# Kernel tuning notes

Hardware: AMD Instinct MI355X
Metric: run time of the kernel (lower is better)

The kernel has to match this reference:

```python
import jax, jax.numpy as jnp
import numpy as np

EPS_COS = 1e-16   # epsilon added to operands (as in the torch module)
EPS_NRM = 1e-8    # torch cosine_similarity clamps norms at 1e-8


def setup_inputs() -> dict:
    key = jax.random.key(0)
    k0, k1, k2, k3, k4, k5 = jax.random.split(key, 6)
    B, N, M = 64, 2048, 256
    stdev = 1.0 / np.sqrt(N + M)
    memory = jax.random.uniform(k0, (B, N, M), jnp.float32, -stdev, stdev)
    k = jax.random.normal(k1, (B, M), jnp.float32)
    g = jax.random.uniform(k2, (B, 1), jnp.float32)
    gamma = jax.random.uniform(k3, (1,), jnp.float32)
    # w_prev[:,0] = w_u_prev, w_prev[:,1] = w_r_prev (positive weightings)
    w_prev = jax.random.uniform(k4, (B, 2, N), jnp.float32)
    # w_lu_prev is a 0/1 least-recently-used mask
    w_lu_prev = jax.random.randint(k5, (B, N), 0, 2, jnp.int32)
    return {"memory": memory, "k": k, "g": g, "gamma": gamma,
            "w_prev": w_prev, "w_lu_prev": w_lu_prev, "n": 4}


def reference(memory, k, g, gamma, w_prev, w_lu_prev, n):
    # --- _similarity: softmax over cosine similarity along memory slots ---
    mem_e = memory + EPS_COS                      # [B, N, M]
    k_e = k[:, None, :] + EPS_COS                 # [B, 1, M]
    num = jnp.einsum('bnm,bom->bn', mem_e, k_e)   # [B, N]
    mem_nrm = jnp.maximum(jnp.linalg.norm(mem_e, axis=-1), EPS_NRM)
    k_nrm = jnp.maximum(jnp.linalg.norm(k_e, axis=-1), EPS_NRM)  # [B, 1]
    w_r = jax.nn.softmax(num / (mem_nrm * k_nrm), axis=-1)       # [B, N]

    # --- interpolate write weighting and usage weighting ---
    w_u_prev = w_prev[:, 0]                        # [B, N]
    w_r_prev = w_prev[:, 1]                        # [B, N]
    w_lu_prev_f = w_lu_prev.astype(memory.dtype)   # [B, N], 0/1 mask
    w_w = g * w_r_prev + (1.0 - g) * w_lu_prev_f   # [B, N]
    w_u = gamma * w_u_prev + w_r + w_w             # [B, N]

    # --- least-used mask: w_u <= n-th smallest usage (per batch) ---
    nth_smallest = jnp.sort(w_u, axis=1)[:, n - 1]           # [B]
    w_lu = (w_u <= nth_smallest[:, None]).astype(memory.dtype)  # [B, N]

    # --- zero out slots that were least-recently-used last step ---
    mem_zeroed = memory * (1.0 - w_lu_prev_f)[..., None]      # [B, N, M]

    # --- lrua_write: rank-1 outer-product write, then read with w_r ---
    mem_new = mem_zeroed + w_w[..., None] * k[:, None, :]     # [B, N, M]
    read = jnp.einsum('bn,bnm->bm', w_r, mem_new)             # [B, M]
    return read
```

## Files before the change

kernel.cpp:

```cpp
#include <hip/hip_runtime.h>
#include <math.h>

#define EPS_COS 1e-16f
#define EPS_NRM 1e-8f

constexpr int B = 64;
constexpr int N = 2048;
constexpr int M = 256;

constexpr int BLK    = 512;
constexpr int WAVES  = BLK / 64;
constexpr int CHUNK  = 256;
constexpr int ROWS   = CHUNK / WAVES;
constexpr int NCHUNK = N / CHUNK;

__global__ __launch_bounds__(BLK)
void k1_fused(const float* __restrict__ mem,
              const float* __restrict__ kk,
              const float* __restrict__ g,
              const float* __restrict__ w_prev,
              const int*   __restrict__ lu_prev,
              float* __restrict__ pread,
              float* __restrict__ pZ,
              float* __restrict__ pS1)
{
    const int b    = blockIdx.y;
    const int c    = blockIdx.x;
    const int tid  = threadIdx.x;
    const int w    = tid >> 6;
    const int lane = tid & 63;
    const int n0   = c * CHUNK;

    float4 kv = *reinterpret_cast<const float4*>(kk + (size_t)b * M + lane * 4);
    kv.x += EPS_COS; kv.y += EPS_COS; kv.z += EPS_COS; kv.w += EPS_COS;
    float ksq = kv.x*kv.x + kv.y*kv.y + kv.z*kv.z + kv.w*kv.w;
#pragma unroll
    for (int off = 32; off; off >>= 1) ksq += __shfl_xor(ksq, off);
    const float kn = fmaxf(sqrtf(ksq), EPS_NRM);

    const float gb   = g[b];
    const float* wrp = w_prev + (size_t)b * 2 * N + N;
    const int*   lup = lu_prev + (size_t)b * N;
    const float* base = mem + ((size_t)b * N + n0 + w) * M + lane * 4;

    float4 acc = make_float4(0.f, 0.f, 0.f, 0.f);
    float Zp = 0.f, s1p = 0.f;

    auto process = [&](int i, const float4& v) {
        float m0 = v.x + EPS_COS, m1 = v.y + EPS_COS;
        float m2 = v.z + EPS_COS, m3 = v.w + EPS_COS;
        float dot = m0*kv.x + m1*kv.y + m2*kv.z + m3*kv.w;
        float msq = m0*m0 + m1*m1 + m2*m2 + m3*m3;
#pragma unroll
        for (int off = 32; off; off >>= 1) {
            dot += __shfl_xor(dot, off);
            msq += __shfl_xor(msq, off);
        }
        const int n = n0 + w + WAVES * i;
        const float cosv = dot / (fmaxf(sqrtf(msq), EPS_NRM) * kn);
        const float e  = __expf(cosv);
        const float lu = (float)lup[n];
        const float ww = gb * wrp[n] + (1.f - gb) * lu;
        Zp += e;
        s1p = fmaf(e, ww, s1p);
        const float cw = e * (1.f - lu);
        acc.x = fmaf(cw, v.x, acc.x);
        acc.y = fmaf(cw, v.y, acc.y);
        acc.z = fmaf(cw, v.z, acc.z);
        acc.w = fmaf(cw, v.w, acc.w);
    };

    float4 cur = *reinterpret_cast<const float4*>(base);
#pragma unroll 4
    for (int i = 0; i < ROWS - 1; ++i) {
        float4 nxt = *reinterpret_cast<const float4*>(base + (size_t)(i + 1) * WAVES * M);
        process(i, cur);
        cur = nxt;
    }
    process(ROWS - 1, cur);

    __shared__ float sred[WAVES * M];
    __shared__ float sZ[WAVES], sS1[WAVES];
    *reinterpret_cast<float4*>(&sred[w * M + lane * 4]) = acc;
    if (lane == 0) { sZ[w] = Zp; sS1[w] = s1p; }
    __syncthreads();

    if (tid < M) {
        float r = 0.f;
#pragma unroll
        for (int q = 0; q < WAVES; ++q) r += sred[q * M + tid];
        pread[((size_t)b * NCHUNK + c) * M + tid] = r;
    }
    if (tid == 0) {
        float z = 0.f, s = 0.f;
#pragma unroll
        for (int q = 0; q < WAVES; ++q) { z += sZ[q]; s += sS1[q]; }
        pZ[b * NCHUNK + c]  = z;
        pS1[b * NCHUNK + c] = s;
    }
}

__global__ __launch_bounds__(M)
void k2_final(const float* __restrict__ pread,
              const float* __restrict__ pZ,
              const float* __restrict__ pS1,
              const float* __restrict__ kk,
              float* __restrict__ out)
{
    const int b = blockIdx.x;
    const int t = threadIdx.x;

    __shared__ float sZ, sS1;
    if (t < 64) {
        float z = (t < NCHUNK) ? pZ[b * NCHUNK + t]  : 0.f;
        float s = (t < NCHUNK) ? pS1[b * NCHUNK + t] : 0.f;
#pragma unroll
        for (int off = 32; off; off >>= 1) {
            z += __shfl_xor(z, off);
            s += __shfl_xor(s, off);
        }
        if (t == 0) { sZ = z; sS1 = s; }
    }
    __syncthreads();

    const float invZ = 1.f / sZ;
    const float* pr = pread + (size_t)b * NCHUNK * M + t;
    float sum = 0.f;
#pragma unroll
    for (int c2 = 0; c2 < NCHUNK; ++c2) sum += pr[(size_t)c2 * M];

    out[(size_t)b * M + t] = (sum + sS1 * kk[(size_t)b * M + t]) * invZ;
}

extern "C" void kernel_launch(void* const* d_in, const int* in_sizes, int n_in,
                              void* d_out, int out_size, void* d_ws, size_t ws_size,
                              hipStream_t stream) {
    const float* mem     = (const float*)d_in[0];
    const float* kk      = (const float*)d_in[1];
    const float* g       = (const float*)d_in[2];
    const float* w_prev  = (const float*)d_in[4];
    const int*   lu_prev = (const int*)  d_in[5];
    float* out = (float*)d_out;

    float* pread = (float*)d_ws;
    float* pZ    = pread + (size_t)B * NCHUNK * M;
    float* pS1   = pZ + (size_t)B * NCHUNK;

    dim3 g1(NCHUNK, B);
    k1_fused<<<g1, BLK, 0, stream>>>(mem, kk, g, w_prev, lu_prev, pread, pZ, pS1);
    k2_final<<<B, M, 0, stream>>>(pread, pZ, pS1, kk, out);
}
```

Baseline: 29.70 us.

## Process two rows per wave with half-wave splits and deeper prefetch

Each wave now splits into two 32-lane halves that each handle a full 256-float row with two float4 loads. This cuts the butterfly shuffle reduction from six steps to five per row and processes two rows per iteration. The block shrinks to 256 threads with 128-row chunks, which doubles the grid and partial outputs, and the software prefetch goes two pairs deep. The cost is more registers, an extra cross-half reduction at the end, and more partials for the final kernel to sum.

After: 29.42 us. About the same (-0.9%).

```diff
diff --git a/kernel.cpp b/kernel.cpp
--- a/kernel.cpp
+++ b/kernel.cpp
@@ -8,10 +8,11 @@
 constexpr int N = 2048;
 constexpr int M = 256;
 
-constexpr int BLK    = 512;
+constexpr int BLK    = 256;
 constexpr int WAVES  = BLK / 64;
-constexpr int CHUNK  = 256;
-constexpr int ROWS   = CHUNK / WAVES;
+constexpr int CHUNK  = 128;
+constexpr int RPW    = CHUNK / WAVES;
+constexpr int PAIRS  = RPW / 2;
 constexpr int NCHUNK = N / CHUNK;
 
 __global__ __launch_bounds__(BLK)
@@ -29,34 +30,45 @@
     const int tid  = threadIdx.x;
     const int w    = tid >> 6;
     const int lane = tid & 63;
-    const int n0   = c * CHUNK;
+    const int half = lane >> 5;
+    const int sub  = lane & 31;
 
-    float4 kv = *reinterpret_cast<const float4*>(kk + (size_t)b * M + lane * 4);
-    kv.x += EPS_COS; kv.y += EPS_COS; kv.z += EPS_COS; kv.w += EPS_COS;
-    float ksq = kv.x*kv.x + kv.y*kv.y + kv.z*kv.z + kv.w*kv.w;
+    float4 ka = *reinterpret_cast<const float4*>(kk + (size_t)b * M + sub * 4);
+    float4 kb = *reinterpret_cast<const float4*>(kk + (size_t)b * M + 128 + sub * 4);
+    ka.x += EPS_COS; ka.y += EPS_COS; ka.z += EPS_COS; ka.w += EPS_COS;
+    kb.x += EPS_COS; kb.y += EPS_COS; kb.z += EPS_COS; kb.w += EPS_COS;
+    float ksq = ka.x*ka.x + ka.y*ka.y + ka.z*ka.z + ka.w*ka.w
+              + kb.x*kb.x + kb.y*kb.y + kb.z*kb.z + kb.w*kb.w;
 #pragma unroll
-    for (int off = 32; off; off >>= 1) ksq += __shfl_xor(ksq, off);
+    for (int off = 16; off; off >>= 1) ksq += __shfl_xor(ksq, off);
     const float kn = fmaxf(sqrtf(ksq), EPS_NRM);
 
     const float gb   = g[b];
     const float* wrp = w_prev + (size_t)b * 2 * N + N;
     const int*   lup = lu_prev + (size_t)b * N;
-    const float* base = mem + ((size_t)b * N + n0 + w) * M + lane * 4;
 
-    float4 acc = make_float4(0.f, 0.f, 0.f, 0.f);
+    const int rowbase = c * CHUNK + w * RPW;
+    const float* p = mem + ((size_t)b * N + rowbase + half) * M + sub * 4;
+
+    float4 accA = make_float4(0.f, 0.f, 0.f, 0.f);
+    float4 accB = make_float4(0.f, 0.f, 0.f, 0.f);
     float Zp = 0.f, s1p = 0.f;
 
-    auto process = [&](int i, const float4& v) {
-        float m0 = v.x + EPS_COS, m1 = v.y + EPS_COS;
-        float m2 = v.z + EPS_COS, m3 = v.w + EPS_COS;
-        float dot = m0*kv.x + m1*kv.y + m2*kv.z + m3*kv.w;
-        float msq = m0*m0 + m1*m1 + m2*m2 + m3*m3;
+    auto process = [&](int i, const float4& va, const float4& vb) {
+        float a0 = va.x + EPS_COS, a1 = va.y + EPS_COS;
+        float a2 = va.z + EPS_COS, a3 = va.w + EPS_COS;
+        float b0 = vb.x + EPS_COS, b1 = vb.y + EPS_COS;
+        float b2 = vb.z + EPS_COS, b3 = vb.w + EPS_COS;
+        float dot = a0*ka.x + a1*ka.y + a2*ka.z + a3*ka.w
+                  + b0*kb.x + b1*kb.y + b2*kb.z + b3*kb.w;
+        float msq = a0*a0 + a1*a1 + a2*a2 + a3*a3
+                  + b0*b0 + b1*b1 + b2*b2 + b3*b3;
 #pragma unroll
-        for (int off = 32; off; off >>= 1) {
+        for (int off = 16; off; off >>= 1) {
             dot += __shfl_xor(dot, off);
             msq += __shfl_xor(msq, off);
         }
-        const int n = n0 + w + WAVES * i;
+        const int n = rowbase + 2 * i + half;
         const float cosv = dot / (fmaxf(sqrtf(msq), EPS_NRM) * kn);
         const float e  = __expf(cosv);
         const float lu = (float)lup[n];
@@ -64,24 +76,44 @@
         Zp += e;
         s1p = fmaf(e, ww, s1p);
         const float cw = e * (1.f - lu);
-        acc.x = fmaf(cw, v.x, acc.x);
-        acc.y = fmaf(cw, v.y, acc.y);
-        acc.z = fmaf(cw, v.z, acc.z);
-        acc.w = fmaf(cw, v.w, acc.w);
+        accA.x = fmaf(cw, va.x, accA.x);
+        accA.y = fmaf(cw, va.y, accA.y);
+        accA.z = fmaf(cw, va.z, accA.z);
+        accA.w = fmaf(cw, va.w, accA.w);
+        accB.x = fmaf(cw, vb.x, accB.x);
+        accB.y = fmaf(cw, vb.y, accB.y);
+        accB.z = fmaf(cw, vb.z, accB.z);
+        accB.w = fmaf(cw, vb.w, accB.w);
     };
 
-    float4 cur = *reinterpret_cast<const float4*>(base);
-#pragma unroll 4
-    for (int i = 0; i < ROWS - 1; ++i) {
-        float4 nxt = *reinterpret_cast<const float4*>(base + (size_t)(i + 1) * WAVES * M);
-        process(i, cur);
-        cur = nxt;
+    float4 va0 = *reinterpret_cast<const float4*>(p);
+    float4 vb0 = *reinterpret_cast<const float4*>(p + 128);
+    float4 va1 = *reinterpret_cast<const float4*>(p + 2 * M);
+    float4 vb1 = *reinterpret_cast<const float4*>(p + 2 * M + 128);
+#pragma unroll 2
+    for (int i = 0; i < PAIRS - 2; ++i) {
+        float4 va2 = *reinterpret_cast<const float4*>(p + (size_t)(i + 2) * 2 * M);
+        float4 vb2 = *reinterpret_cast<const float4*>(p + (size_t)(i + 2) * 2 * M + 128);
+        process(i, va0, vb0);
+        va0 = va1; vb0 = vb1;
+        va1 = va2; vb1 = vb2;
     }
-    process(ROWS - 1, cur);
+    process(PAIRS - 2, va0, vb0);
+    process(PAIRS - 1, va1, vb1);
+
+    accA.x += __shfl_xor(accA.x, 32); accA.y += __shfl_xor(accA.y, 32);
+    accA.z += __shfl_xor(accA.z, 32); accA.w += __shfl_xor(accA.w, 32);
+    accB.x += __shfl_xor(accB.x, 32); accB.y += __shfl_xor(accB.y, 32);
+    accB.z += __shfl_xor(accB.z, 32); accB.w += __shfl_xor(accB.w, 32);
+    Zp  += __shfl_xor(Zp, 32);
+    s1p += __shfl_xor(s1p, 32);
 
     __shared__ float sred[WAVES * M];
     __shared__ float sZ[WAVES], sS1[WAVES];
-    *reinterpret_cast<float4*>(&sred[w * M + lane * 4]) = acc;
+    if (half == 0) {
+        *reinterpret_cast<float4*>(&sred[w * M + sub * 4])       = accA;
+        *reinterpret_cast<float4*>(&sred[w * M + 128 + sub * 4]) = accB;
+    }
     if (lane == 0) { sZ[w] = Zp; sS1[w] = s1p; }
     __syncthreads();
 
```

## Shrink chunks to 64 rows, give each wave contiguous rows with deeper prefetch

Applied to the files above, without the earlier changes.

The first kernel now uses 256-thread blocks over 64-row chunks, so the grid grows from 512 to 2048 blocks. Each wave walks 16 contiguous rows instead of interleaved rows, with a 4-deep register prefetch pipeline. The final kernel has every thread read all 32 partial Z/S1 values directly instead of doing a shared-memory reduction and a barrier. This aims to improve occupancy and memory-level parallelism on the bandwidth-bound pass, at the cost of 4x more partial sums to write and reduce.

New measurement: 34.16 us. +15.0%, slower.

```diff
diff --git a/kernel.cpp b/kernel.cpp
--- a/kernel.cpp
+++ b/kernel.cpp
@@ -8,10 +8,10 @@
 constexpr int N = 2048;
 constexpr int M = 256;
 
-constexpr int BLK    = 512;
+constexpr int BLK    = 256;
 constexpr int WAVES  = BLK / 64;
-constexpr int CHUNK  = 256;
-constexpr int ROWS   = CHUNK / WAVES;
+constexpr int CHUNK  = 64;
+constexpr int RPW    = CHUNK / WAVES;
 constexpr int NCHUNK = N / CHUNK;
 
 __global__ __launch_bounds__(BLK)
@@ -29,7 +29,6 @@
     const int tid  = threadIdx.x;
     const int w    = tid >> 6;
     const int lane = tid & 63;
-    const int n0   = c * CHUNK;
 
     float4 kv = *reinterpret_cast<const float4*>(kk + (size_t)b * M + lane * 4);
     kv.x += EPS_COS; kv.y += EPS_COS; kv.z += EPS_COS; kv.w += EPS_COS;
@@ -41,7 +40,9 @@
     const float gb   = g[b];
     const float* wrp = w_prev + (size_t)b * 2 * N + N;
     const int*   lup = lu_prev + (size_t)b * N;
-    const float* base = mem + ((size_t)b * N + n0 + w) * M + lane * 4;
+
+    const int rowbase = c * CHUNK + w * RPW;
+    const float* p = mem + ((size_t)b * N + rowbase) * M + lane * 4;
 
     float4 acc = make_float4(0.f, 0.f, 0.f, 0.f);
     float Zp = 0.f, s1p = 0.f;
@@ -56,7 +57,7 @@
             dot += __shfl_xor(dot, off);
             msq += __shfl_xor(msq, off);
         }
-        const int n = n0 + w + WAVES * i;
+        const int n = rowbase + i;
         const float cosv = dot / (fmaxf(sqrtf(msq), EPS_NRM) * kn);
         const float e  = __expf(cosv);
         const float lu = (float)lup[n];
@@ -70,14 +71,20 @@
         acc.w = fmaf(cw, v.w, acc.w);
     };
 
-    float4 cur = *reinterpret_cast<const float4*>(base);
-#pragma unroll 4
-    for (int i = 0; i < ROWS - 1; ++i) {
-        float4 nxt = *reinterpret_cast<const float4*>(base + (size_t)(i + 1) * WAVES * M);
-        process(i, cur);
-        cur = nxt;
+    float4 v0 = *reinterpret_cast<const float4*>(p);
+    float4 v1 = *reinterpret_cast<const float4*>(p + (size_t)1 * M);
+    float4 v2 = *reinterpret_cast<const float4*>(p + (size_t)2 * M);
+    float4 v3 = *reinterpret_cast<const float4*>(p + (size_t)3 * M);
+#pragma unroll
+    for (int i = 0; i < RPW - 4; ++i) {
+        float4 v4 = *reinterpret_cast<const float4*>(p + (size_t)(i + 4) * M);
+        process(i, v0);
+        v0 = v1; v1 = v2; v2 = v3; v3 = v4;
     }
-    process(ROWS - 1, cur);
+    process(RPW - 4, v0);
+    process(RPW - 3, v1);
+    process(RPW - 2, v2);
+    process(RPW - 1, v3);
 
     __shared__ float sred[WAVES * M];
     __shared__ float sZ[WAVES], sS1[WAVES];
@@ -85,7 +92,7 @@
     if (lane == 0) { sZ[w] = Zp; sS1[w] = s1p; }
     __syncthreads();
 
-    if (tid < M) {
+    {
         float r = 0.f;
 #pragma unroll
         for (int q = 0; q < WAVES; ++q) r += sred[q * M + tid];
@@ -109,27 +116,17 @@
 {
     const int b = blockIdx.x;
     const int t = threadIdx.x;
-
-    __shared__ float sZ, sS1;
-    if (t < 64) {
-        float z = (t < NCHUNK) ? pZ[b * NCHUNK + t]  : 0.f;
-        float s = (t < NCHUNK) ? pS1[b * NCHUNK + t] : 0.f;
+    float z = 0.f, s = 0.f;
 #pragma unroll
-        for (int off = 32; off; off >>= 1) {
-            z += __shfl_xor(z, off);
-            s += __shfl_xor(s, off);
-        }
-        if (t == 0) { sZ = z; sS1 = s; }
+    for (int q = 0; q < NCHUNK; ++q) {
+        z += pZ[b * NCHUNK + q];
+        s += pS1[b * NCHUNK + q];
     }
-    __syncthreads();
-
-    const float invZ = 1.f / sZ;
     const float* pr = pread + (size_t)b * NCHUNK * M + t;
     float sum = 0.f;
 #pragma unroll
-    for (int c2 = 0; c2 < NCHUNK; ++c2) sum += pr[(size_t)c2 * M];
-
-    out[(size_t)b * M + t] = (sum + sS1 * kk[(size_t)b * M + t]) * invZ;
+    for (int q = 0; q < NCHUNK; ++q) sum += pr[(size_t)q * M];
+    out[(size_t)b * M + t] = (sum + s * kk[(size_t)b * M + t]) / z;
 }
 
 extern "C" void kernel_launch(void* const* d_in, const int* in_sizes, int n_in,
```
